# Optimization experiments

Hardware: AMD Instinct MI355X
Metric: run time of the kernel (lower is better)

The kernel has to match this reference:

```python
import jax, jax.numpy as jnp
import numpy as np

CODEBOOK_SIZE = 8192
CODEBOOK_DIM = 1024
HIDDEN_DIM = 4096
OUT_DIM = 1024
B, M = 32, 576


def setup_inputs() -> dict:
    key = jax.random.key(0)
    k_idx, k_cb, k_w1, k_w2 = jax.random.split(key, 4)
    index = jax.random.randint(k_idx, (B, M), 0, CODEBOOK_SIZE, dtype=jnp.int32)
    # codebook initialized as sqrt(d) * randn, as in the torch module
    codebook = (CODEBOOK_DIM ** 0.5) * jax.random.normal(k_cb, (CODEBOOK_SIZE, CODEBOOK_DIM), dtype=jnp.float32)
    s1 = 1.0 / np.sqrt(CODEBOOK_DIM)
    s2 = 1.0 / np.sqrt(HIDDEN_DIM)
    W1 = s1 * jax.random.normal(k_w1, (CODEBOOK_DIM, HIDDEN_DIM), dtype=jnp.float32)
    b1 = jnp.zeros((HIDDEN_DIM,), dtype=jnp.float32)
    W2 = s2 * jax.random.normal(k_w2, (HIDDEN_DIM, OUT_DIM), dtype=jnp.float32)
    b2 = jnp.zeros((OUT_DIM,), dtype=jnp.float32)
    return {"index": index, "codebook": codebook, "W1": W1, "b1": b1, "W2": W2, "b2": b2}


def reference(index, codebook, W1, b1, W2, b2):
    # one_hot(index) @ codebook is mathematically an index gather:
    # quantized[b, m, :] = codebook[index[b, m], :]
    quantized = jnp.take(codebook, index, axis=0)  # [B, M, D]
    # Decoder_ff: 2-layer GELU MLP (D -> 4D -> D)
    h = jax.nn.gelu(jnp.einsum('bmd,dh->bmh', quantized, W1) + b1)
    rec = jnp.einsum('bmh,ho->bmo', h, W2) + b2
    return rec
```

## Files before the change

### kernel.cpp

```cpp
#include <hip/hip_runtime.h>
#include <stdint.h>

typedef __attribute__((ext_vector_type(8))) short s16x8;
typedef __attribute__((ext_vector_type(4))) float f32x4;

__device__ __forceinline__ short f2bf(float x) {
  uint32_t u = __builtin_bit_cast(uint32_t, x);
  u += 0x7FFFu + ((u >> 16) & 1u);
  return (short)(u >> 16);
}

__device__ __forceinline__ void gload16(void* l, const void* g) {
  __builtin_amdgcn_global_load_lds(
      (const __attribute__((address_space(1))) void*)g,
      (__attribute__((address_space(3))) void*)l, 16, 0, 0);
}

__device__ __forceinline__ float gelu_tanh(float x) {
  float u = 0.7978845608028654f * (x + 0.044715f * x * x * x);
  float e = __expf(2.0f * u);
  return x - x / (e + 1.0f);
}

__global__ void gather_cvt(const float* __restrict__ cb, const int* __restrict__ idx,
                           short* __restrict__ out) {
  int m = blockIdx.x * 2 + (threadIdx.x >> 7);
  int c = (threadIdx.x & 127) * 8;
  const float* s = cb + (size_t)idx[m] * 1024 + c;
  s16x8 o;
#pragma unroll
  for (int j = 0; j < 8; ++j) o[j] = f2bf(s[j]);
  *(s16x8*)(out + (size_t)m * 1024 + c) = o;
}

__global__ void cvt_T(const float* __restrict__ in, short* __restrict__ out, int K, int N) {
  int Kb = K >> 3;
  int t = blockIdx.x * 256 + threadIdx.x;
  if (t >= N * Kb) return;
  int n = t / Kb;
  int k8 = (t - n * Kb) * 8;
  const float* s = in + (size_t)k8 * N + n;
  s16x8 o;
#pragma unroll
  for (int j = 0; j < 8; ++j) o[j] = f2bf(s[(size_t)j * N]);
  *(s16x8*)(out + (size_t)n * K + k8) = o;
}

template <int MODE, int K, int N>
__global__ __launch_bounds__(512, 2) void gemm3b(
    const short* __restrict__ A, const short* __restrict__ Bt,
    const float* __restrict__ bias, void* __restrict__ Cv) {
  constexpr int BM = 144, BN = 256;
  constexpr int ATS = BM * 64;
  constexpr int LDSH = (BM + BN) * 64;
  __shared__ short lds[3 * LDSH + 512];

  constexpr int NBN = N / BN;
  const int nwg = gridDim.x;
  int swz = blockIdx.x;
  swz = (swz & 7) * (nwg >> 3) + (swz >> 3);
  const int bm = swz / NBN, bn = swz - (swz / NBN) * NBN;

  const int tid = threadIdx.x;
  const int wid = tid >> 6, lane = tid & 63;
  const int lr = lane & 15, hi = lane >> 4;

  const int sl = (tid & 7) ^ ((tid >> 3) & 7);
  const long rstep = (long)64 * K;
  const short* aptr0 = A + (long)(bm * BM + (tid >> 3)) * K + sl * 8;
  const short* aptrP = A + (long)(bm * BM + 128 + ((tid >> 3) & 15)) * K + sl * 8;
  const short* bptr0 = Bt + (long)(bn * BN + (tid >> 3)) * K + sl * 8;
  const int wlds = wid * 512;
  const bool realP = (wid < 2);
  constexpr int SCR = 3 * LDSH;

  const int aRB = lr * 64;
  const int bRB = ATS + (wid * 32 + lr) * 64;
  const int sk0 = (hi ^ (lr & 7)) * 8;
  const int sk1 = ((4 + hi) ^ (lr & 7)) * 8;

  f32x4 acc[9][2] = {};
  s16x8 af[5][2], bf[2][2];

  constexpr int NT = K >> 6;

#pragma unroll
  for (int tt = 0; tt < 2; ++tt) {
    const int wb = tt * LDSH, kk = tt * 64;
#pragma unroll
    for (int r = 0; r < 4; ++r) gload16(&lds[wb + ATS + r * 4096 + wlds], bptr0 + r * rstep + kk);
    gload16(&lds[wb + 0 + wlds], aptr0 + kk);
    gload16(&lds[wb + 4096 + wlds], aptr0 + rstep + kk);
    gload16(realP ? &lds[wb + 8192 + wlds] : &lds[SCR], aptrP + kk);
  }
  asm volatile("s_waitcnt vmcnt(7)" ::: "memory");
  __builtin_amdgcn_s_barrier();

  int rb0 = 0, rb1 = LDSH, rb2 = 2 * LDSH;

  for (int t = 0; t < NT; ++t) {
    const int kt = ((t + 2 < NT) ? (t + 2) : t) << 6;

#pragma unroll
    for (int mi = 0; mi < 4; ++mi) {
      af[mi][0] = *(const s16x8*)&lds[rb0 + aRB + mi * 1024 + sk0];
      af[mi][1] = *(const s16x8*)&lds[rb0 + aRB + mi * 1024 + sk1];
    }
#pragma unroll
    for (int nj = 0; nj < 2; ++nj) {
      bf[nj][0] = *(const s16x8*)&lds[rb0 + bRB + nj * 1024 + sk0];
      bf[nj][1] = *(const s16x8*)&lds[rb0 + bRB + nj * 1024 + sk1];
    }
#pragma unroll
    for (int r = 0; r < 4; ++r)
      gload16(&lds[rb2 + ATS + r * 4096 + wlds], bptr0 + r * rstep + kt);
    asm volatile("s_waitcnt lgkmcnt(0)" ::: "memory");
    __builtin_amdgcn_s_setprio(1);
#pragma unroll
    for (int mi = 0; mi < 4; ++mi)
#pragma unroll
      for (int nj = 0; nj < 2; ++nj)
#pragma unroll
        for (int ks = 0; ks < 2; ++ks)
          acc[mi][nj] = __builtin_amdgcn_mfma_f32_16x16x32_bf16(af[mi][ks], bf[nj][ks], acc[mi][nj], 0, 0, 0);
    __builtin_amdgcn_s_setprio(0);

#pragma unroll
    for (int mi = 0; mi < 5; ++mi) {
      af[mi][0] = *(const s16x8*)&lds[rb0 + aRB + (4 + mi) * 1024 + sk0];
      af[mi][1] = *(const s16x8*)&lds[rb0 + aRB + (4 + mi) * 1024 + sk1];
    }
    gload16(&lds[rb2 + 0 + wlds], aptr0 + kt);
    gload16(&lds[rb2 + 4096 + wlds], aptr0 + rstep + kt);
    gload16(realP ? &lds[rb2 + 8192 + wlds] : &lds[SCR], aptrP + kt);
    asm volatile("s_waitcnt lgkmcnt(0)" ::: "memory");
    __builtin_amdgcn_s_setprio(1);
#pragma unroll
    for (int mi = 0; mi < 5; ++mi)
#pragma unroll
      for (int nj = 0; nj < 2; ++nj)
#pragma unroll
        for (int ks = 0; ks < 2; ++ks)
          acc[4 + mi][nj] = __builtin_amdgcn_mfma_f32_16x16x32_bf16(af[mi][ks], bf[nj][ks], acc[4 + mi][nj], 0, 0, 0);
    __builtin_amdgcn_s_setprio(0);

    asm volatile("s_waitcnt vmcnt(7)" ::: "memory");
    __builtin_amdgcn_s_barrier();
    const int tmp = rb0; rb0 = rb1; rb1 = rb2; rb2 = tmp;
  }

  const int m0 = bm * BM + hi * 4;
  const int n0 = bn * BN + wid * 32 + lr;
#pragma unroll
  for (int nj = 0; nj < 2; ++nj) {
    const int n = n0 + nj * 16;
    const float bv = bias[n];
#pragma unroll
    for (int mi = 0; mi < 9; ++mi) {
      f32x4 v = acc[mi][nj];
#pragma unroll
      for (int r = 0; r < 4; ++r) {
        const int m = m0 + mi * 16 + r;
        float x = v[r] + bv;
        if (MODE == 1) {
          ((short*)Cv)[(size_t)m * N + n] = f2bf(gelu_tanh(x));
        } else {
          ((float*)Cv)[(size_t)m * N + n] = x;
        }
      }
    }
  }
}

extern "C" void kernel_launch(void* const* d_in, const int* in_sizes, int n_in,
                              void* d_out, int out_size, void* d_ws, size_t ws_size,
                              hipStream_t stream) {
  const int* idx = (const int*)d_in[0];
  const float* cb = (const float*)d_in[1];
  const float* W1 = (const float*)d_in[2];
  const float* b1 = (const float*)d_in[3];
  const float* W2 = (const float*)d_in[4];
  const float* b2 = (const float*)d_in[5];
  float* out = (float*)d_out;

  const int Mtot = 32 * 576;

  char* ws = (char*)d_ws;
  short* aq = (short*)(ws);
  short* w1t = (short*)(ws + (size_t)40 * 1024 * 1024);
  short* w2t = (short*)(ws + (size_t)48 * 1024 * 1024);
  short* h = (short*)(ws + (size_t)56 * 1024 * 1024);

  gather_cvt<<<Mtot / 2, 256, 0, stream>>>(cb, idx, aq);
  cvt_T<<<2048, 256, 0, stream>>>(W1, w1t, 1024, 4096);
  cvt_T<<<2048, 256, 0, stream>>>(W2, w2t, 4096, 1024);

  size_t avail = (ws_size > (size_t)56 * 1024 * 1024) ? ws_size - (size_t)56 * 1024 * 1024 : 0;
  int nc = 1;
  while (nc < 8 && (size_t)(Mtot / nc) * 8192 > avail) nc <<= 1;
  const int Mc = Mtot / nc;

  for (int c = 0; c < nc; ++c) {
    gemm3b<1, 1024, 4096><<<(Mc / 144) * 16, 512, 0, stream>>>(
        aq + (size_t)c * Mc * 1024, w1t, b1, (void*)h);
    gemm3b<2, 4096, 1024><<<(Mc / 144) * 4, 512, 0, stream>>>(
        h, w2t, b2, (void*)(out + (size_t)c * Mc * 1024));
  }
}
```

Measured before the change: 419.6 us.

## Use 192x256 tiles with 2x4 wave grid and split A/B pipeline depths

Raises the GEMM tile from 144x256 to 192x256 and arranges the eight waves as a 2x4 grid, so each wave computes a 96x64 sub-tile instead of 144x32. This gives each wave a squarer fragment with more operand reuse per LDS read, and removes the padded partial-wave A loads. The A tile now uses double buffering (prefetched one step ahead) while B keeps triple buffering, so the larger tile still fits in LDS. Tile counts become 96 row blocks and the grid sizes change to match. The cost is a shallower prefetch for A and possibly different occupancy or wave balance.

Measured after the change: 436.3 us. 4.0% more time.

```diff
diff --git a/kernel.cpp b/kernel.cpp
--- a/kernel.cpp
+++ b/kernel.cpp
@@ -47,13 +47,14 @@
 }
 
 template <int MODE, int K, int N>
-__global__ __launch_bounds__(512, 2) void gemm3b(
+__global__ __launch_bounds__(512, 2) void gemmk(
     const short* __restrict__ A, const short* __restrict__ Bt,
     const float* __restrict__ bias, void* __restrict__ Cv) {
-  constexpr int BM = 144, BN = 256;
-  constexpr int ATS = BM * 64;
-  constexpr int LDSH = (BM + BN) * 64;
-  __shared__ short lds[3 * LDSH + 512];
+  constexpr int BM = 192, BN = 256;
+  constexpr int AHS = BM * 64;
+  constexpr int BHS = BN * 64;
+  constexpr int BB = 2 * AHS;
+  __shared__ short lds[2 * AHS + 3 * BHS];
 
   constexpr int NBN = N / BN;
   const int nwg = gridDim.x;
@@ -63,100 +64,98 @@
 
   const int tid = threadIdx.x;
   const int wid = tid >> 6, lane = tid & 63;
+  const int wr = wid >> 2, wc = wid & 3;
   const int lr = lane & 15, hi = lane >> 4;
 
   const int sl = (tid & 7) ^ ((tid >> 3) & 7);
   const long rstep = (long)64 * K;
-  const short* aptr0 = A + (long)(bm * BM + (tid >> 3)) * K + sl * 8;
-  const short* aptrP = A + (long)(bm * BM + 128 + ((tid >> 3) & 15)) * K + sl * 8;
-  const short* bptr0 = Bt + (long)(bn * BN + (tid >> 3)) * K + sl * 8;
+  const short* aptr = A + (long)(bm * BM + (tid >> 3)) * K + sl * 8;
+  const short* bptr = Bt + (long)(bn * BN + (tid >> 3)) * K + sl * 8;
   const int wlds = wid * 512;
-  const bool realP = (wid < 2);
-  constexpr int SCR = 3 * LDSH;
-
-  const int aRB = lr * 64;
-  const int bRB = ATS + (wid * 32 + lr) * 64;
+
+  const int aRB = (wr * 96 + lr) * 64;
+  const int bRB = (wc * 64 + lr) * 64;
   const int sk0 = (hi ^ (lr & 7)) * 8;
   const int sk1 = ((4 + hi) ^ (lr & 7)) * 8;
 
-  f32x4 acc[9][2] = {};
-  s16x8 af[5][2], bf[2][2];
+  f32x4 acc[6][4] = {};
+  s16x8 af[3][2], bf[4][2];
 
   constexpr int NT = K >> 6;
 
 #pragma unroll
-  for (int tt = 0; tt < 2; ++tt) {
-    const int wb = tt * LDSH, kk = tt * 64;
-#pragma unroll
-    for (int r = 0; r < 4; ++r) gload16(&lds[wb + ATS + r * 4096 + wlds], bptr0 + r * rstep + kk);
-    gload16(&lds[wb + 0 + wlds], aptr0 + kk);
-    gload16(&lds[wb + 4096 + wlds], aptr0 + rstep + kk);
-    gload16(realP ? &lds[wb + 8192 + wlds] : &lds[SCR], aptrP + kk);
-  }
-  asm volatile("s_waitcnt vmcnt(7)" ::: "memory");
+  for (int r = 0; r < 3; ++r) gload16(&lds[r * 4096 + wlds], aptr + r * rstep);
+#pragma unroll
+  for (int r = 0; r < 4; ++r) gload16(&lds[BB + r * 4096 + wlds], bptr + r * rstep);
+#pragma unroll
+  for (int r = 0; r < 4; ++r) gload16(&lds[BB + BHS + r * 4096 + wlds], bptr + r * rstep + 64);
+  asm volatile("s_waitcnt vmcnt(4)" ::: "memory");
   __builtin_amdgcn_s_barrier();
 
-  int rb0 = 0, rb1 = LDSH, rb2 = 2 * LDSH;
+  int rb0 = BB, rb1 = BB + BHS, rb2 = BB + 2 * BHS;
 
   for (int t = 0; t < NT; ++t) {
-    const int kt = ((t + 2 < NT) ? (t + 2) : t) << 6;
-
-#pragma unroll
-    for (int mi = 0; mi < 4; ++mi) {
-      af[mi][0] = *(const s16x8*)&lds[rb0 + aRB + mi * 1024 + sk0];
-      af[mi][1] = *(const s16x8*)&lds[rb0 + aRB + mi * 1024 + sk1];
-    }
-#pragma unroll
-    for (int nj = 0; nj < 2; ++nj) {
+    const int ca = (t & 1) * AHS;
+    const int na = AHS - ca;
+    const int ka = ((t + 1 < NT) ? (t + 1) : t) << 6;
+    const int kb = ((t + 2 < NT) ? (t + 2) : t) << 6;
+
+#pragma unroll
+    for (int r = 0; r < 3; ++r) gload16(&lds[na + r * 4096 + wlds], aptr + r * rstep + ka);
+
+#pragma unroll
+    for (int mi = 0; mi < 3; ++mi) {
+      af[mi][0] = *(const s16x8*)&lds[ca + aRB + mi * 1024 + sk0];
+      af[mi][1] = *(const s16x8*)&lds[ca + aRB + mi * 1024 + sk1];
+    }
+#pragma unroll
+    for (int nj = 0; nj < 4; ++nj) {
       bf[nj][0] = *(const s16x8*)&lds[rb0 + bRB + nj * 1024 + sk0];
       bf[nj][1] = *(const s16x8*)&lds[rb0 + bRB + nj * 1024 + sk1];
     }
-#pragma unroll
-    for (int r = 0; r < 4; ++r)
-      gload16(&lds[rb2 + ATS + r * 4096 + wlds], bptr0 + r * rstep + kt);
     asm volatile("s_waitcnt lgkmcnt(0)" ::: "memory");
     __builtin_amdgcn_s_setprio(1);
 #pragma unroll
-    for (int mi = 0; mi < 4; ++mi)
-#pragma unroll
-      for (int nj = 0; nj < 2; ++nj)
+    for (int mi = 0; mi < 3; ++mi)
+#pragma unroll
+      for (int nj = 0; nj < 4; ++nj)
 #pragma unroll
         for (int ks = 0; ks < 2; ++ks)
           acc[mi][nj] = __builtin_amdgcn_mfma_f32_16x16x32_bf16(af[mi][ks], bf[nj][ks], acc[mi][nj], 0, 0, 0);
     __builtin_amdgcn_s_setprio(0);
 
 #pragma unroll
-    for (int mi = 0; mi < 5; ++mi) {
-      af[mi][0] = *(const s16x8*)&lds[rb0 + aRB + (4 + mi) * 1024 + sk0];
-      af[mi][1] = *(const s16x8*)&lds[rb0 + aRB + (4 + mi) * 1024 + sk1];
-    }
-    gload16(&lds[rb2 + 0 + wlds], aptr0 + kt);
-    gload16(&lds[rb2 + 4096 + wlds], aptr0 + rstep + kt);
-    gload16(realP ? &lds[rb2 + 8192 + wlds] : &lds[SCR], aptrP + kt);
+    for (int r = 0; r < 4; ++r)
+      gload16(&lds[rb2 + r * 4096 + wlds], bptr + r * rstep + kb);
+#pragma unroll
+    for (int mi = 0; mi < 3; ++mi) {
+      af[mi][0] = *(const s16x8*)&lds[ca + aRB + (3 + mi) * 1024 + sk0];
+      af[mi][1] = *(const s16x8*)&lds[ca + aRB + (3 + mi) * 1024 + sk1];
+    }
     asm volatile("s_waitcnt lgkmcnt(0)" ::: "memory");
     __builtin_amdgcn_s_setprio(1);
 #pragma unroll
-    for (int mi = 0; mi < 5; ++mi)
-#pragma unroll
-      for (int nj = 0; nj < 2; ++nj)
+    for (int mi = 0; mi < 3; ++mi)
+#pragma unroll
+      for (int nj = 0; nj < 4; ++nj)
 #pragma unroll
         for (int ks = 0; ks < 2; ++ks)
-          acc[4 + mi][nj] = __builtin_amdgcn_mfma_f32_16x16x32_bf16(af[mi][ks], bf[nj][ks], acc[4 + mi][nj], 0, 0, 0);
+          acc[3 + mi][nj] = __builtin_amdgcn_mfma_f32_16x16x32_bf16(af[mi][ks], bf[nj][ks], acc[3 + mi][nj], 0, 0, 0);
     __builtin_amdgcn_s_setprio(0);
 
-    asm volatile("s_waitcnt vmcnt(7)" ::: "memory");
+    asm volatile("s_waitcnt vmcnt(4)" ::: "memory");
     __builtin_amdgcn_s_barrier();
     const int tmp = rb0; rb0 = rb1; rb1 = rb2; rb2 = tmp;
   }
 
-  const int m0 = bm * BM + hi * 4;
-  const int n0 = bn * BN + wid * 32 + lr;
-#pragma unroll
-  for (int nj = 0; nj < 2; ++nj) {
+  const int m0 = bm * BM + wr * 96 + hi * 4;
+  const int n0 = bn * BN + wc * 64 + lr;
+#pragma unroll
+  for (int nj = 0; nj < 4; ++nj) {
     const int n = n0 + nj * 16;
     const float bv = bias[n];
 #pragma unroll
-    for (int mi = 0; mi < 9; ++mi) {
+    for (int mi = 0; mi < 6; ++mi) {
       f32x4 v = acc[mi][nj];
 #pragma unroll
       for (int r = 0; r < 4; ++r) {
@@ -201,9 +200,9 @@
   const int Mc = Mtot / nc;
 
   for (int c = 0; c < nc; ++c) {
-    gemm3b<1, 1024, 4096><<<(Mc / 144) * 16, 512, 0, stream>>>(
+    gemmk<1, 1024, 4096><<<(Mc / 192) * 16, 512, 0, stream>>>(
         aq + (size_t)c * Mc * 1024, w1t, b1, (void*)h);
-    gemm3b<2, 4096, 1024><<<(Mc / 144) * 4, 512, 0, stream>>>(
+    gemmk<2, 4096, 1024><<<(Mc / 192) * 4, 512, 0, stream>>>(
         h, w2t, b2, (void*)(out + (size_t)c * Mc * 1024));
   }
 }
```
